# Optimization experiments

Measured on AMD Instinct MI355X. Metric: run time of the kernel, lower is better.

Reference implementation:

```python
import jax, jax.numpy as jnp
import numpy as np
from jax import lax

N, M, B = 512, 1024, 1024  # signal dim, atoms, batch (batch==m required by X = W @ Gamma)
POWER_ITER = 100
IHT_ITER = 50


def setup_inputs() -> dict:
    key = jax.random.key(0)
    k1, k2 = jax.random.split(key)
    Y = jax.random.normal(k1, (B, N), dtype=jnp.float32)
    W = jax.random.normal(k2, (N, M), dtype=jnp.float32)
    return {"Y": Y, "W": W, "K": 64}


def power_method(W):
    # 100 iterations of X <- X W^T W / ||.||; returns last pre-normalization norm
    # (approx largest eigenvalue of W^T W), matching PowerMethod in the source.
    X0 = jax.random.normal(jax.random.key(42), (1, W.shape[1]), dtype=W.dtype)

    def body(i, carry):
        X, _ = carry
        X2 = (X @ W.T) @ W          # [1, m]
        nm = jnp.linalg.norm(X2)
        return (X2 / nm, nm)

    _, nm = lax.fori_loop(0, POWER_ITER, body, (X0, jnp.asarray(1.0, W.dtype)))
    return nm


def hard_threshold_k(G, K):
    # keep entries strictly larger (in abs) than the (K+1)-th largest per row
    a = jnp.sort(jnp.abs(G), axis=1)[:, ::-1]   # descending per row
    T = a[:, K][:, None]                          # [B, 1]
    return G * (jnp.abs(G) > T).astype(G.dtype)


def reference(Y, W, K):
    # NormDict: column-normalize the dictionary
    W = W / jnp.linalg.norm(W, axis=0)
    c = power_method(W)
    eta = 1.0 / c
    Yn = jnp.linalg.norm(Y)

    # IHT sparse coding
    Gamma = hard_threshold_k(Y @ (eta * W), K)     # [B, m]
    residual = Gamma @ W.T - Y                      # [B, n]

    def step(carry, _):
        Gamma, residual = carry
        Gamma = hard_threshold_k(Gamma - eta * (residual @ W), K)
        residual = Gamma @ W.T - Y
        return (Gamma, residual), jnp.linalg.norm(residual) / Yn

    (Gamma, residual), norms = lax.scan(step, (Gamma, residual), None, length=IHT_ITER)

    X = W @ Gamma  # [n, m] @ [B, m] -> requires B == m, as in the torch source
    return X, Gamma, norms
```

## Files before the change

kernel.cpp:

```cpp
#include <hip/hip_runtime.h>


#define DEV __device__ __forceinline__

constexpr int Nd = 512;
constexpr int Md = 1024;
constexpr int Bd = 1024;
constexpr int Ksp = 64;
constexpr int IHT = 50;

DEV float wave_reduce_f(float v) {
#pragma unroll
  for (int off = 32; off > 0; off >>= 1) v += __shfl_down(v, off);
  return v;
}
DEV double wave_reduce_d(double v) {
#pragma unroll
  for (int off = 32; off > 0; off >>= 1) v += __shfl_down(v, off);
  return v;
}
DEV float rfl_f(float v) {
  return __uint_as_float(__builtin_amdgcn_readfirstlane(__float_as_uint(v)));
}

__global__ void k_zero(double* dacc) {
  int t = threadIdx.x;
  if (t < 51) dacc[t] = 0.0;
}

__global__ __launch_bounds__(256) void k_colnorm(const float* __restrict__ W,
                                                 float* __restrict__ cnorm) {
  int col = blockIdx.x * 256 + threadIdx.x;
  double ss = 0.0;
  for (int i = 0; i < Nd; ++i) {
    float w = W[(size_t)i * Md + col];
    ss = fma((double)w, (double)w, ss);
  }
  cnorm[col] = (float)sqrt(ss);
}

__global__ __launch_bounds__(256) void k_normalize(const float* __restrict__ W,
                                                   const float* __restrict__ cnorm,
                                                   float* __restrict__ Wn) {
  int idx = blockIdx.x * 256 + threadIdx.x;
  Wn[idx] = W[idx] / cnorm[idx & (Md - 1)];
}

__global__ __launch_bounds__(256) void k_yn2(const float* __restrict__ Y,
                                             double* __restrict__ dacc) {
  double s = 0.0;
  for (int i = blockIdx.x * 256 + threadIdx.x; i < Bd * Nd; i += gridDim.x * 256) {
    float y = Y[i];
    s = fma((double)y, (double)y, s);
  }
  s = wave_reduce_d(s);
  __shared__ double red[4];
  int lane = threadIdx.x & 63, wid = threadIdx.x >> 6;
  if (lane == 0) red[wid] = s;
  __syncthreads();
  if (threadIdx.x == 0) atomicAdd(&dacc[0], red[0] + red[1] + red[2] + red[3]);
}

template <int BM, int BN, int TN>
__global__ __launch_bounds__(256) void k_gemm_t(const float* __restrict__ A, int lda, int ta,
                                                const float* __restrict__ B, int ldb, int tb,
                                                float* __restrict__ C, int ldc, int Kd,
                                                float scale) {
  constexpr int AE = 32 * BM / 256;
  constexpr int BE = 32 * BN / 256;
  __shared__ __align__(16) float As[32][BM + 4];
  __shared__ __align__(16) float Bs[32][BN + 4];
  const int tid = threadIdx.x;
  const int tx = tid % (BN / TN), ty = tid / (BN / TN);
  const int m0 = blockIdx.y * BM, n0 = blockIdx.x * BN;
  float ra[AE], rb[BE];
  float acc[4][TN];
#pragma unroll
  for (int i = 0; i < 4; ++i)
#pragma unroll
    for (int j = 0; j < TN; ++j) acc[i][j] = 0.f;

  auto loadA = [&](int k0) {
    if (!ta) {
      const int c = tid & 31, r0 = tid >> 5;
#pragma unroll
      for (int i = 0; i < AE; ++i)
        ra[i] = A[(size_t)(m0 + r0 + i * 8) * lda + (k0 + c)];
    } else {
      const int r = tid % BM, c0 = tid / BM;
#pragma unroll
      for (int i = 0; i < AE; ++i)
        ra[i] = A[(size_t)(k0 + c0 + i * (256 / BM)) * lda + (m0 + r)];
    }
  };
  auto storeA = [&]() {
    if (!ta) {
      const int c = tid & 31, r0 = tid >> 5;
#pragma unroll
      for (int i = 0; i < AE; ++i) As[c][r0 + i * 8] = ra[i];
    } else {
      const int r = tid % BM, c0 = tid / BM;
#pragma unroll
      for (int i = 0; i < AE; ++i) As[c0 + i * (256 / BM)][r] = ra[i];
    }
  };
  auto loadB = [&](int k0) {
    if (!tb) {
      const int c = tid % BN, r0 = tid / BN;
#pragma unroll
      for (int i = 0; i < BE; ++i)
        rb[i] = B[(size_t)(k0 + r0 + i * (256 / BN)) * ldb + (n0 + c)];
    } else {
      const int r = tid & 31, c0 = tid >> 5;
#pragma unroll
      for (int i = 0; i < BE; ++i)
        rb[i] = B[(size_t)(n0 + c0 + i * 8) * ldb + (k0 + r)];
    }
  };
  auto storeB = [&]() {
    if (!tb) {
      const int c = tid % BN, r0 = tid / BN;
#pragma unroll
      for (int i = 0; i < BE; ++i) Bs[r0 + i * (256 / BN)][c] = rb[i];
    } else {
      const int r = tid & 31, c0 = tid >> 5;
#pragma unroll
      for (int i = 0; i < BE; ++i) Bs[r][c0 + i * 8] = rb[i];
    }
  };

  loadA(0);
  loadB(0);
  storeA();
  storeB();
  __syncthreads();
  for (int k0 = 0; k0 < Kd; k0 += 32) {
    const bool more = (k0 + 32) < Kd;
    if (more) { loadA(k0 + 32); loadB(k0 + 32); }
#pragma unroll
    for (int kk = 0; kk < 32; ++kk) {
      const float4 a4 = *(const float4*)&As[kk][ty * 4];
      const float aa[4] = {a4.x, a4.y, a4.z, a4.w};
      float bb[TN];
      if constexpr (TN == 4) {
        const float4 b4 = *(const float4*)&Bs[kk][tx * 4];
        bb[0] = b4.x; bb[1] = b4.y; bb[2] = b4.z; bb[3] = b4.w;
      } else {
        const float2 b2 = *(const float2*)&Bs[kk][tx * 2];
        bb[0] = b2.x; bb[1] = b2.y;
      }
#pragma unroll
      for (int i = 0; i < 4; ++i)
#pragma unroll
        for (int j = 0; j < TN; ++j) acc[i][j] = fmaf(aa[i], bb[j], acc[i][j]);
    }
    if (more) {
      __syncthreads();
      storeA();
      storeB();
      __syncthreads();
    }
  }
#pragma unroll
  for (int i = 0; i < 4; ++i) {
    if constexpr (TN == 4) {
      float4 o;
      o.x = acc[i][0] * scale; o.y = acc[i][1] * scale;
      o.z = acc[i][2] * scale; o.w = acc[i][3] * scale;
      *(float4*)&C[(size_t)(m0 + ty * 4 + i) * ldc + n0 + tx * 4] = o;
    } else {
      float2 o;
      o.x = acc[i][0] * scale; o.y = acc[i][1] * scale;
      *(float2*)&C[(size_t)(m0 + ty * 4 + i) * ldc + n0 + tx * 2] = o;
    }
  }
}

DEV float erfinv_xla(float x) {
  float w = -log1pf(-x * x);
  float p;
  if (w < 5.0f) {
    w = w - 2.5f;
    p = 2.81022636e-08f;
    p = fmaf(p, w, 3.43273939e-07f);
    p = fmaf(p, w, -3.5233877e-06f);
    p = fmaf(p, w, -4.39150654e-06f);
    p = fmaf(p, w, 0.00021858087f);
    p = fmaf(p, w, -0.00125372503f);
    p = fmaf(p, w, -0.00417768164f);
    p = fmaf(p, w, 0.246640727f);
    p = fmaf(p, w, 1.50140941f);
  } else {
    w = sqrtf(w) - 3.0f;
    p = -0.000200214257f;
    p = fmaf(p, w, 0.000100950558f);
    p = fmaf(p, w, 0.00134934322f);
    p = fmaf(p, w, -0.00367342844f);
    p = fmaf(p, w, 0.00573950773f);
    p = fmaf(p, w, -0.0076224613f);
    p = fmaf(p, w, 0.00943887047f);
    p = fmaf(p, w, 1.00167406f);
    p = fmaf(p, w, 2.83297682f);
  }
  return p * x;
}

#define TF_ROUND(r)                                  \
  {                                                  \
    x0 += x1;                                        \
    x1 = (x1 << (r)) | (x1 >> (32 - (r)));           \
    x1 ^= x0;                                        \
  }

__global__ void k_x0(float* __restrict__ X0) {
  unsigned i = threadIdx.x;
  unsigned x0 = i, x1 = i + 512u;
  const unsigned ks0 = 0u, ks1 = 42u, ks2 = 0x1BD11BDAu ^ 42u;
  x0 += ks0; x1 += ks1;
  TF_ROUND(13) TF_ROUND(15) TF_ROUND(26) TF_ROUND(6)  x0 += ks1; x1 += ks2 + 1u;
  TF_ROUND(17) TF_ROUND(29) TF_ROUND(16) TF_ROUND(24) x0 += ks2; x1 += ks0 + 2u;
  TF_ROUND(13) TF_ROUND(15) TF_ROUND(26) TF_ROUND(6)  x0 += ks0; x1 += ks1 + 3u;
  TF_ROUND(17) TF_ROUND(29) TF_ROUND(16) TF_ROUND(24) x0 += ks1; x1 += ks2 + 4u;
  TF_ROUND(13) TF_ROUND(15) TF_ROUND(26) TF_ROUND(6)  x0 += ks2; x1 += ks0 + 5u;
  const float lo = -0.99999994f;
  const float sqrt2 = 1.41421356237f;
  {
    float f = __uint_as_float((x0 >> 9) | 0x3f800000u) - 1.0f;
    float u = fmaxf(lo, f * 2.0f + lo);
    X0[i] = sqrt2 * erfinv_xla(u);
  }
  {
    float f = __uint_as_float((x1 >> 9) | 0x3f800000u) - 1.0f;
    float u = fmaxf(lo, f * 2.0f + lo);
    X0[i + 512] = sqrt2 * erfinv_xla(u);
  }
}

__global__ __launch_bounds__(256) void k_z0(const float* __restrict__ X0,
                                            const float* __restrict__ Wn,
                                            float* __restrict__ vout) {
  const int lane = threadIdx.x & 63, wid = threadIdx.x >> 6;
  const int row = blockIdx.x * 4 + wid;
  const float4* wr = (const float4*)(Wn + (size_t)row * Md);
  const float4* x4 = (const float4*)X0;
  float s = 0.f;
#pragma unroll
  for (int e = 0; e < 4; ++e) {
    const float4 w4 = wr[lane + e * 64];
    const float4 xx = x4[lane + e * 64];
    s = fmaf(w4.x, xx.x, s); s = fmaf(w4.y, xx.y, s);
    s = fmaf(w4.z, xx.z, s); s = fmaf(w4.w, xx.w, s);
  }
  s = wave_reduce_f(s);
  if (lane == 0) vout[row] = s;
}

__global__ __launch_bounds__(256) void k_pmv(const float* __restrict__ Mmat,
                                             const float* __restrict__ vin,
                                             float* __restrict__ vout, float scale) {
  const int lane = threadIdx.x & 63, wid = threadIdx.x >> 6;
  const int row = blockIdx.x * 4 + wid;
  const float4* mr = (const float4*)(Mmat + (size_t)row * Nd);
  const float4* v4 = (const float4*)vin;
  float s = 0.f;
#pragma unroll
  for (int e = 0; e < 2; ++e) {
    const float4 m4 = mr[lane + e * 64];
    const float4 xx = v4[lane + e * 64];
    s = fmaf(m4.x, xx.x, s); s = fmaf(m4.y, xx.y, s);
    s = fmaf(m4.z, xx.z, s); s = fmaf(m4.w, xx.w, s);
  }
  s = wave_reduce_f(s);
  if (lane == 0) vout[row] = s * scale;
}

__global__ __launch_bounds__(512) void k_pfinal(const float* __restrict__ v99,
                                                const float* __restrict__ v100,
                                                float* __restrict__ cbuf) {
  __shared__ double r99[8], r100[8];
  const int t = threadIdx.x, lane = t & 63, wid = t >> 6;
  double a = (double)v99[t]; a *= a;
  double b = (double)v100[t]; b *= b;
  a = wave_reduce_d(a);
  b = wave_reduce_d(b);
  if (lane == 0) { r99[wid] = a; r100[wid] = b; }
  __syncthreads();
  if (t == 0) {
    double n99 = 0.0, n100 = 0.0;
    for (int i = 0; i < 8; ++i) { n99 += r99[i]; n100 += r100[i]; }
    float c = (float)(8.0 * sqrt(n100 / n99));
    cbuf[0] = c;
    cbuf[1] = 1.0f / c;
  }
}

__global__ __launch_bounds__(256, 4) void k_iht_all(
    const float* __restrict__ Q, const float* __restrict__ YW,
    const float* __restrict__ cbuf, float* __restrict__ gdense,
    double* __restrict__ normacc) {
  __shared__ float u[Md];
  __shared__ float yws[Md];
  __shared__ float sval[Ksp];
  __shared__ int sidx[Ksp];
  __shared__ unsigned histbuf[2][4][256];
  __shared__ unsigned wred[4];
  __shared__ unsigned sel_need, sel_prefix;
  __shared__ double dred[4];
  __shared__ int scnt;

  const int t = threadIdx.x;
  const int b = blockIdx.x;
  const int lane = t & 63, wv = t >> 6;
  const float eta = cbuf[1];
  const float4 yw = ((const float4*)(YW + (size_t)b * Md))[t];
  ((float4*)yws)[t] = yw;
#pragma unroll
  for (int e = 0; e < 8; ++e) ((unsigned*)histbuf)[t + e * 256] = 0u;
  const float* Qt = Q + t * 4;
  float gdr[4] = {0.f, 0.f, 0.f, 0.f};

  for (int it = -1; it < IHT; ++it) {
    float vals[4];
    unsigned key[4];
    if (it >= 0) {
      const int cnt = scnt;
      float4 p = make_float4(0.f, 0.f, 0.f, 0.f);
      int k = 0;
      for (; k + 16 <= cnt; k += 16) {
#define GROW(j)                                                        \
        const int id##j = __builtin_amdgcn_readfirstlane(sidx[k + j]); \
        const float g##j = rfl_f(sval[k + j]);                         \
        const float4 q##j = *(const float4*)(Qt + (size_t)id##j * Md);
        GROW(0) GROW(1) GROW(2) GROW(3) GROW(4) GROW(5) GROW(6) GROW(7)
        GROW(8) GROW(9) GROW(10) GROW(11) GROW(12) GROW(13) GROW(14) GROW(15)
        p.x = fmaf(g0, q0.x, p.x); p.x = fmaf(g1, q1.x, p.x);
        p.x = fmaf(g2, q2.x, p.x); p.x = fmaf(g3, q3.x, p.x);
        p.x = fmaf(g4, q4.x, p.x); p.x = fmaf(g5, q5.x, p.x);
        p.x = fmaf(g6, q6.x, p.x); p.x = fmaf(g7, q7.x, p.x);
        p.x = fmaf(g8, q8.x, p.x); p.x = fmaf(g9, q9.x, p.x);
        p.x = fmaf(g10, q10.x, p.x); p.x = fmaf(g11, q11.x, p.x);
        p.x = fmaf(g12, q12.x, p.x); p.x = fmaf(g13, q13.x, p.x);
        p.x = fmaf(g14, q14.x, p.x); p.x = fmaf(g15, q15.x, p.x);
        p.y = fmaf(g0, q0.y, p.y); p.y = fmaf(g1, q1.y, p.y);
        p.y = fmaf(g2, q2.y, p.y); p.y = fmaf(g3, q3.y, p.y);
        p.y = fmaf(g4, q4.y, p.y); p.y = fmaf(g5, q5.y, p.y);
        p.y = fmaf(g6, q6.y, p.y); p.y = fmaf(g7, q7.y, p.y);
        p.y = fmaf(g8, q8.y, p.y); p.y = fmaf(g9, q9.y, p.y);
        p.y = fmaf(g10, q10.y, p.y); p.y = fmaf(g11, q11.y, p.y);
        p.y = fmaf(g12, q12.y, p.y); p.y = fmaf(g13, q13.y, p.y);
        p.y = fmaf(g14, q14.y, p.y); p.y = fmaf(g15, q15.y, p.y);
        p.z = fmaf(g0, q0.z, p.z); p.z = fmaf(g1, q1.z, p.z);
        p.z = fmaf(g2, q2.z, p.z); p.z = fmaf(g3, q3.z, p.z);
        p.z = fmaf(g4, q4.z, p.z); p.z = fmaf(g5, q5.z, p.z);
        p.z = fmaf(g6, q6.z, p.z); p.z = fmaf(g7, q7.z, p.z);
        p.z = fmaf(g8, q8.z, p.z); p.z = fmaf(g9, q9.z, p.z);
        p.z = fmaf(g10, q10.z, p.z); p.z = fmaf(g11, q11.z, p.z);
        p.z = fmaf(g12, q12.z, p.z); p.z = fmaf(g13, q13.z, p.z);
        p.z = fmaf(g14, q14.z, p.z); p.z = fmaf(g15, q15.z, p.z);
        p.w = fmaf(g0, q0.w, p.w); p.w = fmaf(g1, q1.w, p.w);
        p.w = fmaf(g2, q2.w, p.w); p.w = fmaf(g3, q3.w, p.w);
        p.w = fmaf(g4, q4.w, p.w); p.w = fmaf(g5, q5.w, p.w);
        p.w = fmaf(g6, q6.w, p.w); p.w = fmaf(g7, q7.w, p.w);
        p.w = fmaf(g8, q8.w, p.w); p.w = fmaf(g9, q9.w, p.w);
        p.w = fmaf(g10, q10.w, p.w); p.w = fmaf(g11, q11.w, p.w);
        p.w = fmaf(g12, q12.w, p.w); p.w = fmaf(g13, q13.w, p.w);
        p.w = fmaf(g14, q14.w, p.w); p.w = fmaf(g15, q15.w, p.w);
#undef GROW
      }
      for (; k + 8 <= cnt; k += 8) {
#define GROW(j)                                                        \
        const int id##j = __builtin_amdgcn_readfirstlane(sidx[k + j]); \
        const float g##j = rfl_f(sval[k + j]);                         \
        const float4 q##j = *(const float4*)(Qt + (size_t)id##j * Md);
        GROW(0) GROW(1) GROW(2) GROW(3) GROW(4) GROW(5) GROW(6) GROW(7)
#undef GROW
        p.x = fmaf(g0, q0.x, p.x); p.x = fmaf(g1, q1.x, p.x);
        p.x = fmaf(g2, q2.x, p.x); p.x = fmaf(g3, q3.x, p.x);
        p.x = fmaf(g4, q4.x, p.x); p.x = fmaf(g5, q5.x, p.x);
        p.x = fmaf(g6, q6.x, p.x); p.x = fmaf(g7, q7.x, p.x);
        p.y = fmaf(g0, q0.y, p.y); p.y = fmaf(g1, q1.y, p.y);
        p.y = fmaf(g2, q2.y, p.y); p.y = fmaf(g3, q3.y, p.y);
        p.y = fmaf(g4, q4.y, p.y); p.y = fmaf(g5, q5.y, p.y);
        p.y = fmaf(g6, q6.y, p.y); p.y = fmaf(g7, q7.y, p.y);
        p.z = fmaf(g0, q0.z, p.z); p.z = fmaf(g1, q1.z, p.z);
        p.z = fmaf(g2, q2.z, p.z); p.z = fmaf(g3, q3.z, p.z);
        p.z = fmaf(g4, q4.z, p.z); p.z = fmaf(g5, q5.z, p.z);
        p.z = fmaf(g6, q6.z, p.z); p.z = fmaf(g7, q7.z, p.z);
        p.w = fmaf(g0, q0.w, p.w); p.w = fmaf(g1, q1.w, p.w);
        p.w = fmaf(g2, q2.w, p.w); p.w = fmaf(g3, q3.w, p.w);
        p.w = fmaf(g4, q4.w, p.w); p.w = fmaf(g5, q5.w, p.w);
        p.w = fmaf(g6, q6.w, p.w); p.w = fmaf(g7, q7.w, p.w);
      }
      for (; k < cnt; ++k) {
        const int id = __builtin_amdgcn_readfirstlane(sidx[k]);
        const float g = rfl_f(sval[k]);
        const float4 q = *(const float4*)(Qt + (size_t)id * Md);
        p.x = fmaf(g, q.x, p.x); p.y = fmaf(g, q.y, p.y);
        p.z = fmaf(g, q.z, p.z); p.w = fmaf(g, q.w, p.w);
      }
      ((float4*)u)[t] = p;
      __syncthreads();
      if (it >= 1) {
        double part = 0.0;
        if (t < cnt) {
          const int id = sidx[t];
          part = (double)sval[t] * ((double)u[id] - 2.0 * (double)yws[id]);
        }
        part = wave_reduce_d(part);
        if (lane == 0) dred[wv] = part;
      }
      __syncthreads();
      if (it >= 1 && t == 0)
        atomicAdd(&normacc[it - 1], dred[0] + dred[1] + dred[2] + dred[3]);
      vals[0] = -(eta * (p.x - yw.x)) + gdr[0];
      vals[1] = -(eta * (p.y - yw.y)) + gdr[1];
      vals[2] = -(eta * (p.z - yw.z)) + gdr[2];
      vals[3] = -(eta * (p.w - yw.w)) + gdr[3];
    } else {
      vals[0] = eta * yw.x; vals[1] = eta * yw.y;
      vals[2] = eta * yw.z; vals[3] = eta * yw.w;
      __syncthreads();
    }
#pragma unroll
    for (int e = 0; e < 4; ++e) key[e] = __float_as_uint(vals[e]) & 0x7fffffffu;

    unsigned need = Ksp + 1, prefix = 0u, pmask = 0u;
#pragma unroll
    for (int pass = 3; pass >= 0; --pass) {
      const int sh = 8 * pass;
      const int pb = pass & 1;
      unsigned(*hist)[256] = histbuf[pb];
#pragma unroll
      for (int e = 0; e < 4; ++e)
        if ((key[e] & pmask) == prefix) atomicAdd(&hist[wv][(key[e] >> sh) & 255u], 1u);
      __syncthreads();
      unsigned* hz = histbuf[pb ^ 1][wv];
      hz[lane] = 0u; hz[lane + 64] = 0u; hz[lane + 128] = 0u; hz[lane + 192] = 0u;
      if (wv == 0) {
        const unsigned c0 = hist[0][lane] + hist[1][lane] + hist[2][lane] + hist[3][lane];
        const unsigned c1 = hist[0][lane + 64] + hist[1][lane + 64] + hist[2][lane + 64] + hist[3][lane + 64];
        const unsigned c2 = hist[0][lane + 128] + hist[1][lane + 128] + hist[2][lane + 128] + hist[3][lane + 128];
        const unsigned c3 = hist[0][lane + 192] + hist[1][lane + 192] + hist[2][lane + 192] + hist[3][lane + 192];
        unsigned s0 = c0, s1 = c1, s2 = c2, s3 = c3;
#pragma unroll
        for (int off = 1; off < 64; off <<= 1) {
          const unsigned y0 = __shfl_down(s0, off), y1 = __shfl_down(s1, off);
          const unsigned y2 = __shfl_down(s2, off), y3 = __shfl_down(s3, off);
          if (lane + off < 64) { s0 += y0; s1 += y1; s2 += y2; s3 += y3; }
        }
        const unsigned T1 = __builtin_amdgcn_readfirstlane(s1);
        const unsigned T2 = __builtin_amdgcn_readfirstlane(s2);
        const unsigned T3 = __builtin_amdgcn_readfirstlane(s3);
        const unsigned i0 = s0 + T1 + T2 + T3;
        const unsigned i1 = s1 + T2 + T3;
        const unsigned i2 = s2 + T3;
        const unsigned i3 = s3;
        if (i0 >= need && i0 - c0 < need) { sel_prefix = prefix | ((unsigned)lane << sh); sel_need = need - (i0 - c0); }
        if (i1 >= need && i1 - c1 < need) { sel_prefix = prefix | ((unsigned)(lane + 64) << sh); sel_need = need - (i1 - c1); }
        if (i2 >= need && i2 - c2 < need) { sel_prefix = prefix | ((unsigned)(lane + 128) << sh); sel_need = need - (i2 - c2); }
        if (i3 >= need && i3 - c3 < need) { sel_prefix = prefix | ((unsigned)(lane + 192) << sh); sel_need = need - (i3 - c3); }
      }
      __syncthreads();
      prefix = sel_prefix;
      need = sel_need;
      pmask |= (255u << sh);
    }
    const unsigned Tbits = prefix;

    unsigned keep = 0u;
    unsigned myc = 0u;
#pragma unroll
    for (int e = 0; e < 4; ++e)
      if (key[e] > Tbits) { keep |= (1u << e); ++myc; }
    gdr[0] = (keep & 1u) ? vals[0] : 0.f;
    gdr[1] = (keep & 2u) ? vals[1] : 0.f;
    gdr[2] = (keep & 4u) ? vals[2] : 0.f;
    gdr[3] = (keep & 8u) ? vals[3] : 0.f;
    unsigned x = myc;
#pragma unroll
    for (int off = 1; off < 64; off <<= 1) {
      const unsigned y = __shfl_up(x, off);
      if (lane >= off) x += y;
    }
    if (lane == 63) wred[wv] = x;
    __syncthreads();
    unsigned addlo = 0u;
    for (int w2 = 0; w2 < wv; ++w2) addlo += wred[w2];
    int base = (int)(x + addlo) - (int)myc;
#pragma unroll
    for (int e = 0; e < 4; ++e) {
      if (keep & (1u << e)) {
        sidx[base] = t * 4 + e;
        sval[base] = vals[e];
        ++base;
      }
    }
    if (t == 0) scnt = (int)(wred[0] + wred[1] + wred[2] + wred[3]);
    if (it == IHT - 1) {
      float4 g;
      g.x = gdr[0]; g.y = gdr[1]; g.z = gdr[2]; g.w = gdr[3];
      ((float4*)(gdense + (size_t)b * Md))[t] = g;
    }
    __syncthreads();
  }

  const int cnt = scnt;
  if (wv == 0) {
    double part = 0.0;
    if (lane < cnt) {
      const int id = sidx[lane];
      float acc2 = 0.f;
      for (int k = 0; k < cnt; ++k)
        acc2 = fmaf(sval[k], Q[(size_t)sidx[k] * Md + id], acc2);
      part = (double)sval[lane] * ((double)acc2 - 2.0 * (double)yws[id]);
    }
    part = wave_reduce_d(part);
    if (lane == 0) atomicAdd(&normacc[IHT - 1], part);
  }
}

__global__ void k_wnorms(const double* __restrict__ dacc, float* __restrict__ onorms) {
  const int t = threadIdx.x;
  if (t < IHT) {
    const double yn2 = dacc[0];
    double r2 = yn2 + dacc[1 + t];
    if (r2 < 0.0) r2 = 0.0;
    onorms[t] = (float)(sqrt(r2) / sqrt(yn2));
  }
}

extern "C" void kernel_launch(void* const* d_in, const int* in_sizes, int n_in,
                              void* d_out, int out_size, void* d_ws, size_t ws_size,
                              hipStream_t stream) {
  (void)in_sizes; (void)n_in; (void)out_size; (void)ws_size;
  const float* Y = (const float*)d_in[0];
  const float* W = (const float*)d_in[1];
  float* out = (float*)d_out;
  float* outX = out;
  float* outG = out + Nd * Md;
  float* outN = outG + Bd * Md;

  char* wsb = (char*)d_ws;
  double* dacc = (double*)wsb;
  float* cbuf = (float*)(wsb + 512);
  float* Wn = (float*)(wsb + 1024);
  float* Q = Wn + Nd * Md;
  float* YW = Q + Md * Md;
  float* Smat = YW + Bd * Md;
  float* S2 = Smat + Nd * Nd;
  float* cnorm = S2 + Nd * Nd;
  float* X0 = cnorm + Md;
  float* V = X0 + Md;

  k_zero<<<1, 64, 0, stream>>>(dacc);
  k_colnorm<<<4, 256, 0, stream>>>(W, cnorm);
  k_normalize<<<2048, 256, 0, stream>>>(W, cnorm, Wn);

  k_gemm_t<64, 32, 2><<<dim3(16, 8), 256, 0, stream>>>(Wn, Md, 0, Wn, Md, 1, Smat, Nd, Md, 1.0f);
  k_gemm_t<64, 32, 2><<<dim3(16, 8), 256, 0, stream>>>(Smat, Nd, 0, Smat, Nd, 0, S2, Nd, Nd, 0.015625f);
  k_gemm_t<64, 64, 4><<<dim3(16, 16), 256, 0, stream>>>(Wn, Md, 1, Wn, Md, 0, Q, Md, Nd, 1.0f);
  k_gemm_t<64, 64, 4><<<dim3(16, 16), 256, 0, stream>>>(Y, Nd, 0, Wn, Md, 0, YW, Md, Nd, 1.0f);
  k_yn2<<<128, 256, 0, stream>>>(Y, dacc);

  k_x0<<<1, 512, 0, stream>>>(X0);
  k_z0<<<128, 256, 0, stream>>>(X0, Wn, V);
  float* pin = V;
  float* pout = V + 512;
  for (int i = 0; i < 49; ++i) {
    k_pmv<<<128, 256, 0, stream>>>(S2, pin, pout, 1.0f);
    float* tp = pin; pin = pout; pout = tp;
  }
  k_pmv<<<128, 256, 0, stream>>>(Smat, pin, V + 1024, 0.125f);
  k_pmv<<<128, 256, 0, stream>>>(Smat, V + 1024, V + 1536, 0.125f);
  k_pfinal<<<1, 512, 0, stream>>>(V + 1024, V + 1536, cbuf);

  k_iht_all<<<1024, 256, 0, stream>>>(Q, YW, cbuf, outG, dacc + 1);
  k_wnorms<<<1, 64, 0, stream>>>(dacc, outN);

  k_gemm_t<64, 32, 2><<<dim3(32, 8), 256, 0, stream>>>(Wn, Md, 0, outG, Md, 0, outX, Md, Md, 1.0f);
}
```

Measured before the change: 945.8 us.

## Refine top-K threshold radix select in a single wave using compacted candidates

Runs only the first 8-bit radix pass as a block-wide histogram. The keys that fall in the selected bin are compacted into shared memory, and the remaining three passes run inside one wavefront using ballot and shuffle instead of block barriers. This cuts the per-iteration __syncthreads count for the hard threshold across the 50 IHT iterations. The cost is that the other waves sit idle while wave 0 works, and the wave is serialized if many keys land in the chosen bin.

Measured after the change: 986.3 us. 4.3% more time.

```diff
diff --git a/kernel.cpp b/kernel.cpp
--- a/kernel.cpp
+++ b/kernel.cpp
@@ -302,9 +302,13 @@
   __shared__ float yws[Md];
   __shared__ float sval[Ksp];
   __shared__ int sidx[Ksp];
-  __shared__ unsigned histbuf[2][4][256];
+  __shared__ unsigned hist8[4][256];
+  __shared__ unsigned cand[Md];
+  __shared__ unsigned h256[256];
   __shared__ unsigned wred[4];
-  __shared__ unsigned sel_need, sel_prefix;
+  __shared__ unsigned sel_bin, sel_need1;
+  __shared__ unsigned tbits_s;
+  __shared__ unsigned ccount;
   __shared__ double dred[4];
   __shared__ int scnt;
 
@@ -315,7 +319,7 @@
   const float4 yw = ((const float4*)(YW + (size_t)b * Md))[t];
   ((float4*)yws)[t] = yw;
 #pragma unroll
-  for (int e = 0; e < 8; ++e) ((unsigned*)histbuf)[t + e * 256] = 0u;
+  for (int e = 0; e < 4; ++e) ((unsigned*)hist8)[t + e * 256] = 0u;
   const float* Qt = Q + t * 4;
   float gdr[4] = {0.f, 0.f, 0.f, 0.f};
 
@@ -424,23 +428,66 @@
 #pragma unroll
     for (int e = 0; e < 4; ++e) key[e] = __float_as_uint(vals[e]) & 0x7fffffffu;
 
-    unsigned need = Ksp + 1, prefix = 0u, pmask = 0u;
-#pragma unroll
-    for (int pass = 3; pass >= 0; --pass) {
-      const int sh = 8 * pass;
-      const int pb = pass & 1;
-      unsigned(*hist)[256] = histbuf[pb];
-#pragma unroll
-      for (int e = 0; e < 4; ++e)
-        if ((key[e] & pmask) == prefix) atomicAdd(&hist[wv][(key[e] >> sh) & 255u], 1u);
-      __syncthreads();
-      unsigned* hz = histbuf[pb ^ 1][wv];
+#pragma unroll
+    for (int e = 0; e < 4; ++e) atomicAdd(&hist8[wv][key[e] >> 24], 1u);
+    if (t == 0) ccount = 0u;
+    __syncthreads();
+    if (wv == 0) {
+      const unsigned c0 = hist8[0][lane] + hist8[1][lane] + hist8[2][lane] + hist8[3][lane];
+      const unsigned c1 = hist8[0][lane + 64] + hist8[1][lane + 64] + hist8[2][lane + 64] + hist8[3][lane + 64];
+      const unsigned c2 = hist8[0][lane + 128] + hist8[1][lane + 128] + hist8[2][lane + 128] + hist8[3][lane + 128];
+      const unsigned c3 = hist8[0][lane + 192] + hist8[1][lane + 192] + hist8[2][lane + 192] + hist8[3][lane + 192];
+      unsigned s0 = c0, s1 = c1, s2 = c2, s3 = c3;
+#pragma unroll
+      for (int off = 1; off < 64; off <<= 1) {
+        const unsigned y0 = __shfl_down(s0, off), y1 = __shfl_down(s1, off);
+        const unsigned y2 = __shfl_down(s2, off), y3 = __shfl_down(s3, off);
+        if (lane + off < 64) { s0 += y0; s1 += y1; s2 += y2; s3 += y3; }
+      }
+      const unsigned T1 = __builtin_amdgcn_readfirstlane(s1);
+      const unsigned T2 = __builtin_amdgcn_readfirstlane(s2);
+      const unsigned T3 = __builtin_amdgcn_readfirstlane(s3);
+      const unsigned i0 = s0 + T1 + T2 + T3;
+      const unsigned i1 = s1 + T2 + T3;
+      const unsigned i2 = s2 + T3;
+      const unsigned i3 = s3;
+      const unsigned need = Ksp + 1;
+      if (i0 >= need && i0 - c0 < need) { sel_bin = (unsigned)lane; sel_need1 = need - (i0 - c0); }
+      if (i1 >= need && i1 - c1 < need) { sel_bin = (unsigned)(lane + 64); sel_need1 = need - (i1 - c1); }
+      if (i2 >= need && i2 - c2 < need) { sel_bin = (unsigned)(lane + 128); sel_need1 = need - (i2 - c2); }
+      if (i3 >= need && i3 - c3 < need) { sel_bin = (unsigned)(lane + 192); sel_need1 = need - (i3 - c3); }
+    }
+    __syncthreads();
+    {
+      const unsigned sb = sel_bin;
+#pragma unroll
+      for (int e = 0; e < 4; ++e) {
+        if ((key[e] >> 24) == sb) {
+          const unsigned pos = atomicAdd(&ccount, 1u);
+          cand[pos] = key[e];
+        }
+      }
+      unsigned* hz = hist8[wv];
       hz[lane] = 0u; hz[lane + 64] = 0u; hz[lane + 128] = 0u; hz[lane + 192] = 0u;
-      if (wv == 0) {
-        const unsigned c0 = hist[0][lane] + hist[1][lane] + hist[2][lane] + hist[3][lane];
-        const unsigned c1 = hist[0][lane + 64] + hist[1][lane + 64] + hist[2][lane + 64] + hist[3][lane + 64];
-        const unsigned c2 = hist[0][lane + 128] + hist[1][lane + 128] + hist[2][lane + 128] + hist[3][lane + 128];
-        const unsigned c3 = hist[0][lane + 192] + hist[1][lane + 192] + hist[2][lane + 192] + hist[3][lane + 192];
+    }
+    __syncthreads();
+    if (wv == 0) {
+      unsigned prefix = sel_bin << 24;
+      unsigned need = sel_need1;
+      unsigned pmask = 0xFF000000u;
+      const int c = (int)ccount;
+#pragma unroll
+      for (int ps = 0; ps < 3; ++ps) {
+        const int sh = 16 - 8 * ps;
+        h256[lane] = 0u; h256[lane + 64] = 0u; h256[lane + 128] = 0u; h256[lane + 192] = 0u;
+        __threadfence_block();
+        for (int i = lane; i < c; i += 64) {
+          const unsigned kk = cand[i];
+          if ((kk & pmask) == prefix) atomicAdd(&h256[(kk >> sh) & 255u], 1u);
+        }
+        __threadfence_block();
+        const unsigned c0 = h256[lane], c1 = h256[lane + 64];
+        const unsigned c2 = h256[lane + 128], c3 = h256[lane + 192];
         unsigned s0 = c0, s1 = c1, s2 = c2, s3 = c3;
 #pragma unroll
         for (int off = 1; off < 64; off <<= 1) {
@@ -455,17 +502,22 @@
         const unsigned i1 = s1 + T2 + T3;
         const unsigned i2 = s2 + T3;
         const unsigned i3 = s3;
-        if (i0 >= need && i0 - c0 < need) { sel_prefix = prefix | ((unsigned)lane << sh); sel_need = need - (i0 - c0); }
-        if (i1 >= need && i1 - c1 < need) { sel_prefix = prefix | ((unsigned)(lane + 64) << sh); sel_need = need - (i1 - c1); }
-        if (i2 >= need && i2 - c2 < need) { sel_prefix = prefix | ((unsigned)(lane + 128) << sh); sel_need = need - (i2 - c2); }
-        if (i3 >= need && i3 - c3 < need) { sel_prefix = prefix | ((unsigned)(lane + 192) << sh); sel_need = need - (i3 - c3); }
-      }
-      __syncthreads();
-      prefix = sel_prefix;
-      need = sel_need;
-      pmask |= (255u << sh);
-    }
-    const unsigned Tbits = prefix;
+        unsigned npfx = 0u, nneed = 0u;
+        bool flag = false;
+        if (i0 >= need && i0 - c0 < need) { npfx = prefix | ((unsigned)lane << sh); nneed = need - (i0 - c0); flag = true; }
+        if (i1 >= need && i1 - c1 < need) { npfx = prefix | ((unsigned)(lane + 64) << sh); nneed = need - (i1 - c1); flag = true; }
+        if (i2 >= need && i2 - c2 < need) { npfx = prefix | ((unsigned)(lane + 128) << sh); nneed = need - (i2 - c2); flag = true; }
+        if (i3 >= need && i3 - c3 < need) { npfx = prefix | ((unsigned)(lane + 192) << sh); nneed = need - (i3 - c3); flag = true; }
+        const unsigned long long mv = __ballot(flag);
+        const int src = __ffsll((long long)mv) - 1;
+        prefix = __shfl(npfx, src);
+        need = __shfl(nneed, src);
+        pmask |= (255u << sh);
+      }
+      if (lane == 0) tbits_s = prefix;
+    }
+    __syncthreads();
+    const unsigned Tbits = tbits_s;
 
     unsigned keep = 0u;
     unsigned myc = 0u;
```
